# Kernel tuning notes

Hardware: AMD Instinct MI355X
Metric: run time of the kernel (lower is better)

## Reference

```python
import jax, jax.numpy as jnp
import numpy as np
import math

B, S, D, H, L, DFF = 64, 512, 512, 8, 2, 1024
DK = D // H
NEG = -1e32
LN_EPS = 1e-5


def cosine_pos_emb(seqlen, d_model):
    # pe[:,0::2]=sin(pos*div), pe[:,1::2]=cos(pos*div) -- fully overwrites the randn init
    pos = jnp.arange(seqlen, dtype=jnp.float32)[:, None]
    div = jnp.exp(jnp.arange(0, d_model, 2, dtype=jnp.float32) * (-math.log(10000.0) / d_model))
    ang = pos * div  # [S, D/2]
    return jnp.stack([jnp.sin(ang), jnp.cos(ang)], axis=-1).reshape(seqlen, d_model)


def layernorm(x, g, b):
    m = jnp.mean(x, axis=-1, keepdims=True)
    v = jnp.var(x, axis=-1, keepdims=True)
    return g * (x - m) * jax.lax.rsqrt(v + LN_EPS) + b


def setup_inputs() -> dict:
    key = jax.random.key(0)
    ks = jax.random.split(key, 8)
    sc = 0.02
    inp = {
        'q_embed_data': jax.random.normal(ks[0], (B, S, D), jnp.float32),
        'qa_embed_data': jax.random.normal(ks[1], (B, S, D), jnp.float32),
        'forget_rate': jax.random.uniform(ks[2], (B, 1, S, 1), jnp.float32),
        # per-block params, leading dim = n_blocks (kq_same=1: q uses k_linear)
        'Wk': jax.random.normal(ks[3], (L, D, D), jnp.float32) * sc,
        'bk': jnp.zeros((L, D), jnp.float32),
        'Wv': jax.random.normal(ks[4], (L, D, D), jnp.float32) * sc,
        'bv': jnp.zeros((L, D), jnp.float32),
        'Wo': jax.random.normal(ks[5], (L, D, D), jnp.float32) * sc,
        'bo': jnp.zeros((L, D), jnp.float32),
        'ln1_g': jnp.ones((L, D), jnp.float32),
        'ln1_b': jnp.zeros((L, D), jnp.float32),
        'W1': jax.random.normal(ks[6], (L, D, DFF), jnp.float32) * sc,
        'b1': jnp.zeros((L, DFF), jnp.float32),
        'W2': jax.random.normal(ks[7], (L, DFF, D), jnp.float32) * sc,
        'b2': jnp.zeros((L, D), jnp.float32),
        'ln2_g': jnp.ones((L, D), jnp.float32),
        'ln2_b': jnp.zeros((L, D), jnp.float32),
    }
    return inp


def reference(q_embed_data, qa_embed_data, forget_rate, Wk, bk, Wv, bv, Wo, bo,
              ln1_g, ln1_b, W1, b1, W2, b2, ln2_g, ln2_b):
    pe = cosine_pos_emb(S, D)
    x = q_embed_data + pe  # query/key stream
    y = qa_embed_data + pe  # value stream (fixed across blocks)
    # mask=0 path: np.triu(ones, k=0) == 0 -> strictly lower-triangular allowed
    allow = jnp.tril(jnp.ones((S, S), dtype=bool), -1)
    scale = 1.0 / math.sqrt(DK)
    for i in range(L):
        qk = (x @ Wk[i] + bk[i]).reshape(B, S, H, DK).transpose(0, 2, 1, 3)  # [B,H,S,dk]
        v = (y @ Wv[i] + bv[i]).reshape(B, S, H, DK).transpose(0, 2, 1, 3)
        scores = jnp.einsum('bhqd,bhkd->bhqk', qk, qk) * scale
        scores = scores * forget_rate  # [B,1,S,1] broadcasts over heads and keys
        scores = jnp.where(allow, scores, NEG)
        p = jax.nn.softmax(scores, axis=-1)
        p = p.at[:, :, 0, :].set(0.0)  # zero_pad: first query row zeroed
        attn = jnp.einsum('bhqk,bhkd->bhqd', p, v).transpose(0, 2, 1, 3).reshape(B, S, D)
        attn = attn @ Wo[i] + bo[i]
        x = layernorm(x + attn, ln1_g[i], ln1_b[i])
        ff = jax.nn.relu(x @ W1[i] + b1[i]) @ W2[i] + b2[i]
        x = layernorm(x + ff, ln2_g[i], ln2_b[i])
    return x
```

## Files before the change

kernel.cpp:

```cpp
#include <hip/hip_runtime.h>
#include <cstdio>

#define B_   64
#define S_   512
#define D_   512
#define H_   8
#define DK_  64
#define DFF_ 1024
#define L_   2
#define BS_  (B_ * S_)

typedef __attribute__((ext_vector_type(8))) short bf16x8;
typedef __attribute__((ext_vector_type(4))) short bf16x4;
typedef __attribute__((ext_vector_type(4))) float f32x4;

__device__ inline short f2bf(float f) {
  unsigned u = __float_as_uint(f);
  u = u + 0x7FFF + ((u >> 16) & 1);
  return (short)(u >> 16);
}
__device__ inline float bf2f(short s) {
  return __uint_as_float(((unsigned)(unsigned short)s) << 16);
}

__device__ inline void gl_lds16(const short* g, void* lds_base) {
  __builtin_amdgcn_global_load_lds(
      (const __attribute__((address_space(1))) void*)g,
      (__attribute__((address_space(3))) void*)lds_base, 16, 0, 0);
}

__global__ void pe_kernel(float* __restrict__ pe) {
  int idx = blockIdx.x * 256 + threadIdx.x;
  int s = idx >> 9, d = idx & 511;
  float dv = __expf((float)(d & ~1) * (-9.210340371976184f / (float)D_));
  float ang = (float)s * dv;
  pe[idx] = (d & 1) ? cosf(ang) : sinf(ang);
}

__global__ __launch_bounds__(256) void prep_kernel(
    const float* __restrict__ q, const float* __restrict__ qa,
    const float* __restrict__ pe, float* __restrict__ x,
    short* __restrict__ xb, short* __restrict__ yb) {
  size_t base = ((size_t)blockIdx.x * 256 + threadIdx.x) * 8;
  int sd = (int)(base & (size_t)(S_ * D_ - 1));
  f32x4 p0 = *(const f32x4*)(pe + sd);
  f32x4 p1 = *(const f32x4*)(pe + sd + 4);
  f32x4 q0 = *(const f32x4*)(q + base);
  f32x4 q1 = *(const f32x4*)(q + base + 4);
  f32x4 a0 = *(const f32x4*)(qa + base);
  f32x4 a1 = *(const f32x4*)(qa + base + 4);
  f32x4 x0, x1; bf16x8 xv, yv;
#pragma unroll
  for (int i = 0; i < 4; ++i) {
    float xe = q0[i] + p0[i]; x0[i] = xe; xv[i] = f2bf(xe);
    yv[i] = f2bf(a0[i] + p0[i]);
  }
#pragma unroll
  for (int i = 0; i < 4; ++i) {
    float xe = q1[i] + p1[i]; x1[i] = xe; xv[4 + i] = f2bf(xe);
    yv[4 + i] = f2bf(a1[i] + p1[i]);
  }
  *(f32x4*)(x + base) = x0;
  *(f32x4*)(x + base + 4) = x1;
  *(bf16x8*)(xb + base) = xv;
  *(bf16x8*)(yb + base) = yv;
}

struct TrArgs {
  const float* src[10];
  short* dst[10];
  int R[10], C[10];
};
__global__ __launch_bounds__(256) void tr_w_all(TrArgs a) {
  const int slot = blockIdx.z;
  const int R = a.R[slot], C = a.C[slot];
  const int c0 = blockIdx.x * 64, r0 = blockIdx.y * 64;
  if (c0 >= C || r0 >= R) return;
  const float* __restrict__ src = a.src[slot];
  short* __restrict__ dst = a.dst[slot];
  __shared__ short Ts[64][72];
  const int t = threadIdx.x;
#pragma unroll
  for (int it = 0; it < 2; ++it) {
    int c2 = it * 256 + t;
    int srow = c2 >> 3, schunk = c2 & 7;
    const float* sp = src + (size_t)(r0 + srow) * C + c0 + schunk * 8;
    f32x4 a0 = *(const f32x4*)sp;
    f32x4 a1 = *(const f32x4*)(sp + 4);
#pragma unroll
    for (int k = 0; k < 4; ++k) Ts[srow][schunk * 8 + k] = f2bf(a0[k]);
#pragma unroll
    for (int k = 0; k < 4; ++k) Ts[srow][schunk * 8 + 4 + k] = f2bf(a1[k]);
  }
  __syncthreads();
#pragma unroll
  for (int it = 0; it < 2; ++it) {
    int c2 = it * 256 + t;
    int orow = c2 >> 3, ochunk = c2 & 7;
    bf16x8 vv;
#pragma unroll
    for (int k = 0; k < 8; ++k) vv[k] = Ts[ochunk * 8 + k][orow];
    *(bf16x8*)(dst + (size_t)(c0 + orow) * R + r0 + ochunk * 8) = vv;
  }
}

__global__ __launch_bounds__(256, 2) void gemm_bt(
    const short* __restrict__ A, const short* __restrict__ BT,
    const float* __restrict__ bias, short* __restrict__ Cb,
    int M, int N, int K, int relu, int bias_row, int nx, int xmaj)
{
  const int nwg = gridDim.x;
  const int cpx = nwg >> 3;
  const int l = (blockIdx.x & 7) * cpx + (blockIdx.x >> 3);
  int bcol, brow;
  if (xmaj) { bcol = l % nx; brow = l / nx; }
  else      { int ny = nwg / nx; brow = l % ny; bcol = l / ny; }

  __shared__ __align__(16) short As[2][128][32];
  __shared__ __align__(16) short Bs[2][256][32];
  const int t = threadIdx.x;
  const int w = t >> 6, lane = t & 63, lr = lane & 15, lk = lane >> 4;
  const int wr = w >> 1, wc = w & 1;

  const f32x4 vzero = {0.f, 0.f, 0.f, 0.f};
  f32x4 acc[4][8];
#pragma unroll
  for (int m = 0; m < 4; ++m)
#pragma unroll
    for (int n = 0; n < 8; ++n) acc[m][n] = vzero;

  const short* Abase = A + (size_t)brow * 128 * K;
  const short* Bbase = BT + (size_t)bcol * 256 * K;

  auto stage = [&](int buf, int k0) {
#pragma unroll
    for (int it = 0; it < 2; ++it) {
      int cb = it * 256 + w * 64;
      int c = cb + lane;
      gl_lds16(Abase + (size_t)(c >> 2) * K + k0 + (c & 3) * 8, (char*)&As[buf][0][0] + (size_t)cb * 16);
    }
#pragma unroll
    for (int it = 0; it < 4; ++it) {
      int cb = it * 256 + w * 64;
      int c = cb + lane;
      gl_lds16(Bbase + (size_t)(c >> 2) * K + k0 + (c & 3) * 8, (char*)&Bs[buf][0][0] + (size_t)cb * 16);
    }
  };

  stage(0, 0);
  int cur = 0;
  for (int k0 = 0; k0 < K; k0 += 32) {
    if (k0 + 32 < K) {
      stage(cur ^ 1, k0 + 32);
      asm volatile("s_waitcnt vmcnt(6)" ::: "memory");
    } else {
      asm volatile("s_waitcnt vmcnt(0)" ::: "memory");
    }
    asm volatile("s_barrier" ::: "memory");

    bf16x8 af[4], bf[8];
#pragma unroll
    for (int m = 0; m < 4; ++m) af[m] = *(const bf16x8*)&As[cur][wr * 64 + m * 16 + lr][lk * 8];
#pragma unroll
    for (int n = 0; n < 8; ++n) bf[n] = *(const bf16x8*)&Bs[cur][wc * 128 + n * 16 + lr][lk * 8];
#pragma unroll
    for (int m = 0; m < 4; ++m)
#pragma unroll
      for (int n = 0; n < 8; ++n)
        acc[m][n] = __builtin_amdgcn_mfma_f32_16x16x32_bf16(bf[n], af[m], acc[m][n], 0, 0, 0);

    asm volatile("s_barrier" ::: "memory");
    cur ^= 1;
  }

#pragma unroll
  for (int m = 0; m < 4; ++m) {
    int row = brow * 128 + wr * 64 + m * 16 + lr;
    float brv = (bias && bias_row) ? bias[row] : 0.f;
    size_t rb = (size_t)row * N;
#pragma unroll
    for (int n = 0; n < 8; ++n) {
      int colb = bcol * 256 + wc * 128 + n * 16 + lk * 4;
      f32x4 bv4;
      if (bias && !bias_row) bv4 = *(const f32x4*)(bias + colb);
      else { bv4[0] = brv; bv4[1] = brv; bv4[2] = brv; bv4[3] = brv; }
      bf16x4 ov;
#pragma unroll
      for (int j = 0; j < 4; ++j) {
        float vv = acc[m][n][j] + bv4[j];
        if (relu) vv = fmaxf(vv, 0.f);
        ov[j] = f2bf(vv);
      }
      *(bf16x4*)(Cb + rb + colb) = ov;
    }
  }
}

template<int P>
__device__ __forceinline__ void attn_body(
    const short* __restrict__ qk, const short* __restrict__ vT,
    const float* __restrict__ fr, short* __restrict__ out,
    short (*Pl)[552], float (*redsum)[32][4],
    int h, int b, int w, int lr, int lk)
{
  constexpr int qo0 = 32 * P, qo1 = 32 * (15 - P);
  constexpr int c0 = 2 * P + 2;
  constexpr int colb1 = c0 * 16;

  const size_t qk_head = (size_t)b * S_ * D_ + (size_t)h * DK_;
  const float scale = 0.125f;

  bf16x8 qf0[2][2], qf1[2][2];
#pragma unroll
  for (int qt = 0; qt < 2; ++qt)
#pragma unroll
    for (int ks = 0; ks < 2; ++ks) {
      qf0[qt][ks] = *(const bf16x8*)(qk + qk_head + (size_t)(qo0 + qt * 16 + lr) * D_ + ks * 32 + lk * 8);
      qf1[qt][ks] = *(const bf16x8*)(qk + qk_head + (size_t)(qo1 + qt * 16 + lr) * D_ + ks * 32 + lk * 8);
    }

  float frv0[2], frv1[2];
#pragma unroll
  for (int qt = 0; qt < 2; ++qt) {
    frv0[qt] = scale * fr[(size_t)b * S_ + qo0 + qt * 16 + lr];
    frv1[qt] = scale * fr[(size_t)b * S_ + qo1 + qt * 16 + lr];
  }

  const f32x4 vzero = {0.f, 0.f, 0.f, 0.f};
  f32x4 acc[9][2];
#pragma unroll
  for (int i = 0; i < 9; ++i) { acc[i][0] = vzero; acc[i][1] = vzero; }

  const int nfr = (w < 2) ? 9 : 8;
  const short* kqbase = qk + qk_head + (size_t)lr * D_ + lk * 8;
  auto kfoff = [&](int i) -> size_t {
    int f = w + 4 * i;
    int kt = (f < c0) ? f : f - c0;
    return (size_t)kt * 16 * D_;
  };
  bf16x8 kbuf[2][2];
  {
    const short* p = kqbase + kfoff(0);
    kbuf[0][0] = *(const bf16x8*)p;
    kbuf[0][1] = *(const bf16x8*)(p + 32);
  }
#pragma unroll
  for (int i = 0; i < 9; ++i) {
    if (i < nfr) {
      if (i + 1 < nfr) {
        const short* p = kqbase + kfoff(i + 1);
        kbuf[(i + 1) & 1][0] = *(const bf16x8*)p;
        kbuf[(i + 1) & 1][1] = *(const bf16x8*)(p + 32);
      }
      const int f = w + 4 * i;
      if (f < c0) {
#pragma unroll
        for (int ks = 0; ks < 2; ++ks) {
          acc[i][0] = __builtin_amdgcn_mfma_f32_16x16x32_bf16(kbuf[i & 1][ks], qf0[0][ks], acc[i][0], 0, 0, 0);
          acc[i][1] = __builtin_amdgcn_mfma_f32_16x16x32_bf16(kbuf[i & 1][ks], qf0[1][ks], acc[i][1], 0, 0, 0);
        }
      } else {
#pragma unroll
        for (int ks = 0; ks < 2; ++ks) {
          acc[i][0] = __builtin_amdgcn_mfma_f32_16x16x32_bf16(kbuf[i & 1][ks], qf1[0][ks], acc[i][0], 0, 0, 0);
          acc[i][1] = __builtin_amdgcn_mfma_f32_16x16x32_bf16(kbuf[i & 1][ks], qf1[1][ks], acc[i][1], 0, 0, 0);
        }
      }
    }
  }

  float rs00 = 0.f, rs01 = 0.f, rs10 = 0.f, rs11 = 0.f;
#pragma unroll
  for (int frag = 0; frag < 34; ++frag) {
    if ((frag & 3) == w) {
      const int i = frag >> 2;
      const int tl = (frag < c0) ? 0 : 1;
      const int kt = tl ? frag - c0 : frag;
      const int kbase = kt * 16 + lk * 4;
      const int colb = (tl ? colb1 : 0) + kbase;
#pragma unroll
      for (int qt = 0; qt < 2; ++qt) {
        int qrow = (tl ? qo1 : qo0) + qt * 16 + lr;
        float fv = tl ? frv1[qt] : frv0[qt];
        bf16x4 pk;
        float rs = 0.f;
#pragma unroll
        for (int j = 0; j < 4; ++j) {
          float e = (kbase + j < qrow) ? __expf(acc[i][qt][j] * fv) : 0.f;
          rs += e;
          pk[j] = f2bf(e);
        }
        *(bf16x4*)&Pl[qt * 16 + lr][colb] = pk;
        if (tl == 0) { if (qt == 0) rs00 += rs; else rs01 += rs; }
        else         { if (qt == 0) rs10 += rs; else rs11 += rs; }
      }
    }
  }

#pragma unroll
  for (int msk = 16; msk < 64; msk <<= 1) {
    rs00 += __shfl_xor(rs00, msk);
    rs01 += __shfl_xor(rs01, msk);
    rs10 += __shfl_xor(rs10, msk);
    rs11 += __shfl_xor(rs11, msk);
  }
  if (lk == 0) {
    redsum[0][lr][w] = rs00;
    redsum[0][16 + lr][w] = rs01;
    redsum[1][lr][w] = rs10;
    redsum[1][16 + lr][w] = rs11;
  }
  __syncthreads();

  const int uqt0 = w & 1, udh0 = w >> 1;
  const int uqt1 = w >> 1, udh1 = w & 1;
  const short* vu0 = vT + (size_t)(h * DK_ + udh0 * 32 + lr) * BS_ + (size_t)b * S_ + lk * 8;
  const short* vu1 = vT + (size_t)(h * DK_ + udh1 * 32 + lr) * BS_ + (size_t)b * S_ + lk * 8;
  const short* prow0 = &Pl[uqt0 * 16 + lr][lk * 8];
  const short* prow1 = &Pl[uqt1 * 16 + lr][colb1 + lk * 8];

  f32x4 oacc0[2] = {vzero, vzero}, oacc1[2] = {vzero, vzero};
  bf16x8 paB[2][2];
  bf16x8 vfB[2][2][2];
  paB[0][0] = *(const bf16x8*)prow0;
  paB[0][1] = *(const bf16x8*)prow1;
#pragma unroll
  for (int n = 0; n < 2; ++n) {
    vfB[0][0][n] = *(const bf16x8*)(vu0 + (size_t)n * 16 * BS_);
    vfB[0][1][n] = *(const bf16x8*)(vu1 + (size_t)n * 16 * BS_);
  }
#pragma unroll
  for (int kb = 0; kb < 16; ++kb) {
    const int pc = kb & 1, pn = (kb + 1) & 1;
    if (kb + 1 < P + 1) {
      paB[pn][0] = *(const bf16x8*)(prow0 + (kb + 1) * 32);
#pragma unroll
      for (int n = 0; n < 2; ++n)
        vfB[pn][0][n] = *(const bf16x8*)(vu0 + (size_t)n * 16 * BS_ + (kb + 1) * 32);
    }
    if (kb + 1 < 16 - P) {
      paB[pn][1] = *(const bf16x8*)(prow1 + (kb + 1) * 32);
#pragma unroll
      for (int n = 0; n < 2; ++n)
        vfB[pn][1][n] = *(const bf16x8*)(vu1 + (size_t)n * 16 * BS_ + (kb + 1) * 32);
    }
    if (kb < P + 1) {
#pragma unroll
      for (int n = 0; n < 2; ++n)
        oacc0[n] = __builtin_amdgcn_mfma_f32_16x16x32_bf16(paB[pc][0], vfB[pc][0][n], oacc0[n], 0, 0, 0);
    }
    if (kb < 16 - P) {
#pragma unroll
      for (int n = 0; n < 2; ++n)
        oacc1[n] = __builtin_amdgcn_mfma_f32_16x16x32_bf16(paB[pc][1], vfB[pc][1][n], oacc1[n], 0, 0, 0);
    }
  }

  {
    float invd[4];
#pragma unroll
    for (int j = 0; j < 4; ++j) {
      int row = uqt0 * 16 + lk * 4 + j;
      float ds = redsum[0][row][0] + redsum[0][row][1] + redsum[0][row][2] + redsum[0][row][3];
      invd[j] = ds > 0.f ? 1.f / ds : 0.f;
    }
#pragma unroll
    for (int n = 0; n < 2; ++n)
#pragma unroll
      for (int j = 0; j < 4; ++j) {
        int qrow = qo0 + uqt0 * 16 + lk * 4 + j;
        out[qk_head + (size_t)qrow * D_ + udh0 * 32 + n * 16 + lr] = f2bf(oacc0[n][j] * invd[j]);
      }
  }
  {
    float invd[4];
#pragma unroll
    for (int j = 0; j < 4; ++j) {
      int row = uqt1 * 16 + lk * 4 + j;
      float ds = redsum[1][row][0] + redsum[1][row][1] + redsum[1][row][2] + redsum[1][row][3];
      invd[j] = ds > 0.f ? 1.f / ds : 0.f;
    }
#pragma unroll
    for (int n = 0; n < 2; ++n)
#pragma unroll
      for (int j = 0; j < 4; ++j) {
        int qrow = qo1 + uqt1 * 16 + lk * 4 + j;
        out[qk_head + (size_t)qrow * D_ + udh1 * 32 + n * 16 + lr] = f2bf(oacc1[n][j] * invd[j]);
      }
  }
}

__global__ __launch_bounds__(256, 3) void attn_kernel(
    const short* __restrict__ qk, const short* __restrict__ vT,
    const float* __restrict__ fr, short* __restrict__ out)
{
  const int hw = blockIdx.x;
  const int l = (hw & 7) * 512 + (hw >> 3);
  const int p = l & 7, hb = l >> 3;
  const int h = hb & 7, b = hb >> 3;
  const int t = threadIdx.x;
  const int w = t >> 6, lr = t & 15, lk = (t & 63) >> 4;

  __shared__ short Pl[32][552];
  __shared__ float redsum[2][32][4];

  switch (p) {
    case 0: attn_body<0>(qk, vT, fr, out, Pl, redsum, h, b, w, lr, lk); break;
    case 1: attn_body<1>(qk, vT, fr, out, Pl, redsum, h, b, w, lr, lk); break;
    case 2: attn_body<2>(qk, vT, fr, out, Pl, redsum, h, b, w, lr, lk); break;
    case 3: attn_body<3>(qk, vT, fr, out, Pl, redsum, h, b, w, lr, lk); break;
    case 4: attn_body<4>(qk, vT, fr, out, Pl, redsum, h, b, w, lr, lk); break;
    case 5: attn_body<5>(qk, vT, fr, out, Pl, redsum, h, b, w, lr, lk); break;
    case 6: attn_body<6>(qk, vT, fr, out, Pl, redsum, h, b, w, lr, lk); break;
    case 7: attn_body<7>(qk, vT, fr, out, Pl, redsum, h, b, w, lr, lk); break;
  }
}

__global__ __launch_bounds__(256) void ln_res(
    const float* __restrict__ xin, const short* __restrict__ add,
    const float* __restrict__ g, const float* __restrict__ bb,
    float* __restrict__ xout, short* __restrict__ xbout)
{
  const int row = blockIdx.x * 4 + (threadIdx.x >> 6);
  const int lane = threadIdx.x & 63;
  const size_t base = (size_t)row * D_ + lane * 8;

  f32x4 a0 = *(const f32x4*)(xin + base);
  f32x4 a1 = *(const f32x4*)(xin + base + 4);
  bf16x8 av = *(const bf16x8*)(add + base);
  float vals[8];
#pragma unroll
  for (int i = 0; i < 4; ++i) vals[i] = a0[i] + bf2f(av[i]);
#pragma unroll
  for (int i = 0; i < 4; ++i) vals[4 + i] = a1[i] + bf2f(av[4 + i]);

  float s = 0.f, sq = 0.f;
#pragma unroll
  for (int i = 0; i < 8; ++i) { s += vals[i]; sq += vals[i] * vals[i]; }
#pragma unroll
  for (int m = 1; m < 64; m <<= 1) { s += __shfl_xor(s, m); sq += __shfl_xor(sq, m); }

  float mean = s * (1.f / D_);
  float var = sq * (1.f / D_) - mean * mean;
  float rstd = rsqrtf(var + 1e-5f);

  int col = lane * 8;
  f32x4 o0, o1; bf16x8 ob;
#pragma unroll
  for (int i = 0; i < 8; ++i) {
    float vv = g[col + i] * (vals[i] - mean) * rstd + bb[col + i];
    if (i < 4) o0[i] = vv; else o1[i - 4] = vv;
    ob[i] = f2bf(vv);
  }
  *(f32x4*)(xout + base) = o0;
  *(f32x4*)(xout + base + 4) = o1;
  *(bf16x8*)(xbout + base) = ob;
}

extern "C" void kernel_launch(void* const* d_in, const int* in_sizes, int n_in,
                              void* d_out, int out_size, void* d_ws, size_t ws_size,
                              hipStream_t stream) {
  const float* q_emb = (const float*)d_in[0];
  const float* qa_emb = (const float*)d_in[1];
  const float* frate = (const float*)d_in[2];
  const float* Wk = (const float*)d_in[3];
  const float* bk = (const float*)d_in[4];
  const float* Wv = (const float*)d_in[5];
  const float* bv = (const float*)d_in[6];
  const float* Wo = (const float*)d_in[7];
  const float* bo = (const float*)d_in[8];
  const float* ln1g = (const float*)d_in[9];
  const float* ln1b = (const float*)d_in[10];
  const float* W1 = (const float*)d_in[11];
  const float* b1 = (const float*)d_in[12];
  const float* W2 = (const float*)d_in[13];
  const float* b2 = (const float*)d_in[14];
  const float* ln2g = (const float*)d_in[15];
  const float* ln2b = (const float*)d_in[16];
  float* x = (float*)d_out;

  char* ws = (char*)d_ws;
  size_t off = 0;
  auto alloc = [&](size_t bytes) -> void* {
    void* p = ws + off;
    off += (bytes + 255) & ~(size_t)255;
    return p;
  };
  const size_t MTOK = (size_t)BS_;
  float* pe    = (float*)alloc((size_t)S_ * D_ * 4);
  short* xb    = (short*)alloc(MTOK * D_ * 2);
  short* yb    = (short*)alloc(MTOK * D_ * 2);
  short* qkb   = (short*)alloc(MTOK * D_ * 2);
  short* vTb   = (short*)alloc(MTOK * D_ * 2);
  short* ff1b  = (short*)alloc(MTOK * DFF_ * 2);
  short* attnb = ff1b;
  short* goutb = qkb;
  short* wT[L_][5];
  for (int i = 0; i < L_; ++i) {
    wT[i][0] = (short*)alloc((size_t)D_ * D_ * 2);
    wT[i][1] = (short*)alloc((size_t)D_ * D_ * 2);
    wT[i][2] = (short*)alloc((size_t)D_ * D_ * 2);
    wT[i][3] = (short*)alloc((size_t)D_ * DFF_ * 2);
    wT[i][4] = (short*)alloc((size_t)DFF_ * D_ * 2);
  }
  if (off > ws_size) {
    fprintf(stderr, "parKT: workspace overflow: need %zu have %zu\n", off, ws_size);
    return;
  }

  pe_kernel<<<(S_ * D_) / 256, 256, 0, stream>>>(pe);
  prep_kernel<<<(int)(MTOK * D_ / (256 * 8)), 256, 0, stream>>>(q_emb, qa_emb, pe, x, xb, yb);

  TrArgs ta;
  for (int i = 0; i < L_; ++i) {
    ta.src[i * 5 + 0] = Wk + (size_t)i * D_ * D_;  ta.dst[i * 5 + 0] = wT[i][0]; ta.R[i * 5 + 0] = D_;   ta.C[i * 5 + 0] = D_;
    ta.src[i * 5 + 1] = Wv + (size_t)i * D_ * D_;  ta.dst[i * 5 + 1] = wT[i][1]; ta.R[i * 5 + 1] = D_;   ta.C[i * 5 + 1] = D_;
    ta.src[i * 5 + 2] = Wo + (size_t)i * D_ * D_;  ta.dst[i * 5 + 2] = wT[i][2]; ta.R[i * 5 + 2] = D_;   ta.C[i * 5 + 2] = D_;
    ta.src[i * 5 + 3] = W1 + (size_t)i * D_ * DFF_; ta.dst[i * 5 + 3] = wT[i][3]; ta.R[i * 5 + 3] = D_;   ta.C[i * 5 + 3] = DFF_;
    ta.src[i * 5 + 4] = W2 + (size_t)i * DFF_ * D_; ta.dst[i * 5 + 4] = wT[i][4]; ta.R[i * 5 + 4] = DFF_; ta.C[i * 5 + 4] = D_;
  }
  tr_w_all<<<dim3(DFF_ / 64, DFF_ / 64, 10), 256, 0, stream>>>(ta);

  const int M = (int)MTOK;
  for (int i = 0; i < L_; ++i) {
    gemm_bt<<<(M / 128) * (D_ / 256), 256, 0, stream>>>(xb, wT[i][0], bk + (size_t)i * D_, qkb, M, D_, D_, 0, 0, D_ / 256, 1);
    gemm_bt<<<(D_ / 128) * (M / 256), 256, 0, stream>>>(wT[i][1], yb, bv + (size_t)i * D_, vTb, D_, M, D_, 0, 1, M / 256, 0);
    attn_kernel<<<(S_ / 64) * H_ * B_, 256, 0, stream>>>(qkb, vTb, frate, attnb);
    gemm_bt<<<(M / 128) * (D_ / 256), 256, 0, stream>>>(attnb, wT[i][2], bo + (size_t)i * D_, goutb, M, D_, D_, 0, 0, D_ / 256, 1);
    ln_res<<<M / 4, 256, 0, stream>>>(x, goutb, ln1g + (size_t)i * D_, ln1b + (size_t)i * D_, x, xb);
    gemm_bt<<<(M / 128) * (DFF_ / 256), 256, 0, stream>>>(xb, wT[i][3], b1 + (size_t)i * DFF_, ff1b, M, DFF_, D_, 1, 0, DFF_ / 256, 1);
    gemm_bt<<<(M / 128) * (D_ / 256), 256, 0, stream>>>(ff1b, wT[i][4], b2 + (size_t)i * D_, goutb, M, D_, DFF_, 0, 0, D_ / 256, 1);
    ln_res<<<M / 4, 256, 0, stream>>>(x, goutb, ln2g + (size_t)i * D_, ln2b + (size_t)i * D_, x, xb);
  }
}
```

Before: 815.2 us.

## Carry residual stream in bf16 and prefetch V earlier in attention

Removes the fp32 residual copy of x: prep no longer writes it, and the layernorm kernels read and write only the bf16 activation, except the last one, which emits fp32 output. This cuts large fp32 read/write traffic in every residual layernorm. Separately, the attention kernel hoists V fragment loads ahead of the softmax phase and adds sched barriers to overlap loads with MFMA. The risk is reduced precision, because the residual is accumulated in bf16.

```diff
diff --git a/kernel.cpp b/kernel.cpp
--- a/kernel.cpp
+++ b/kernel.cpp
@@ -39,7 +39,7 @@
 
 __global__ __launch_bounds__(256) void prep_kernel(
     const float* __restrict__ q, const float* __restrict__ qa,
-    const float* __restrict__ pe, float* __restrict__ x,
+    const float* __restrict__ pe,
     short* __restrict__ xb, short* __restrict__ yb) {
   size_t base = ((size_t)blockIdx.x * 256 + threadIdx.x) * 8;
   int sd = (int)(base & (size_t)(S_ * D_ - 1));
@@ -49,19 +49,17 @@
   f32x4 q1 = *(const f32x4*)(q + base + 4);
   f32x4 a0 = *(const f32x4*)(qa + base);
   f32x4 a1 = *(const f32x4*)(qa + base + 4);
-  f32x4 x0, x1; bf16x8 xv, yv;
+  bf16x8 xv, yv;
 #pragma unroll
   for (int i = 0; i < 4; ++i) {
-    float xe = q0[i] + p0[i]; x0[i] = xe; xv[i] = f2bf(xe);
+    xv[i] = f2bf(q0[i] + p0[i]);
     yv[i] = f2bf(a0[i] + p0[i]);
   }
 #pragma unroll
   for (int i = 0; i < 4; ++i) {
-    float xe = q1[i] + p1[i]; x1[i] = xe; xv[4 + i] = f2bf(xe);
+    xv[4 + i] = f2bf(q1[i] + p1[i]);
     yv[4 + i] = f2bf(a1[i] + p1[i]);
   }
-  *(f32x4*)(x + base) = x0;
-  *(f32x4*)(x + base + 4) = x1;
   *(bf16x8*)(xb + base) = xv;
   *(bf16x8*)(yb + base) = yv;
 }
@@ -206,6 +204,8 @@
   constexpr int qo0 = 32 * P, qo1 = 32 * (15 - P);
   constexpr int c0 = 2 * P + 2;
   constexpr int colb1 = c0 * 16;
+  constexpr int n0 = P + 1;
+  constexpr int n1 = 16 - P;
 
   const size_t qk_head = (size_t)b * S_ * D_ + (size_t)h * DK_;
   const float scale = 0.125f;
@@ -252,6 +252,7 @@
         kbuf[(i + 1) & 1][0] = *(const bf16x8*)p;
         kbuf[(i + 1) & 1][1] = *(const bf16x8*)(p + 32);
       }
+      __builtin_amdgcn_sched_barrier(0);
       const int f = w + 4 * i;
       if (f < c0) {
 #pragma unroll
@@ -266,8 +267,29 @@
           acc[i][1] = __builtin_amdgcn_mfma_f32_16x16x32_bf16(kbuf[i & 1][ks], qf1[1][ks], acc[i][1], 0, 0, 0);
         }
       }
-    }
-  }
+      __builtin_amdgcn_sched_barrier(0);
+    }
+  }
+
+  const int uqt0 = w & 1, udh0 = w >> 1;
+  const int uqt1 = w >> 1, udh1 = w & 1;
+  const short* vu0 = vT + (size_t)(h * DK_ + udh0 * 32 + lr) * BS_ + (size_t)b * S_ + lk * 8;
+  const short* vu1 = vT + (size_t)(h * DK_ + udh1 * 32 + lr) * BS_ + (size_t)b * S_ + lk * 8;
+  bf16x8 vfB[2][2][2];
+#pragma unroll
+  for (int n = 0; n < 2; ++n) {
+    vfB[0][0][n] = *(const bf16x8*)(vu0 + (size_t)n * 16 * BS_);
+    vfB[0][1][n] = *(const bf16x8*)(vu1 + (size_t)n * 16 * BS_);
+  }
+  if (1 < n0) {
+#pragma unroll
+    for (int n = 0; n < 2; ++n)
+      vfB[1][0][n] = *(const bf16x8*)(vu0 + (size_t)n * 16 * BS_ + 32);
+  }
+#pragma unroll
+  for (int n = 0; n < 2; ++n)
+    vfB[1][1][n] = *(const bf16x8*)(vu1 + (size_t)n * 16 * BS_ + 32);
+  __builtin_amdgcn_sched_barrier(0);
 
   float rs00 = 0.f, rs01 = 0.f, rs10 = 0.f, rs11 = 0.f;
 #pragma unroll
@@ -312,48 +334,41 @@
   }
   __syncthreads();
 
-  const int uqt0 = w & 1, udh0 = w >> 1;
-  const int uqt1 = w >> 1, udh1 = w & 1;
-  const short* vu0 = vT + (size_t)(h * DK_ + udh0 * 32 + lr) * BS_ + (size_t)b * S_ + lk * 8;
-  const short* vu1 = vT + (size_t)(h * DK_ + udh1 * 32 + lr) * BS_ + (size_t)b * S_ + lk * 8;
   const short* prow0 = &Pl[uqt0 * 16 + lr][lk * 8];
   const short* prow1 = &Pl[uqt1 * 16 + lr][colb1 + lk * 8];
-
   f32x4 oacc0[2] = {vzero, vzero}, oacc1[2] = {vzero, vzero};
   bf16x8 paB[2][2];
-  bf16x8 vfB[2][2][2];
   paB[0][0] = *(const bf16x8*)prow0;
   paB[0][1] = *(const bf16x8*)prow1;
-#pragma unroll
-  for (int n = 0; n < 2; ++n) {
-    vfB[0][0][n] = *(const bf16x8*)(vu0 + (size_t)n * 16 * BS_);
-    vfB[0][1][n] = *(const bf16x8*)(vu1 + (size_t)n * 16 * BS_);
-  }
+
 #pragma unroll
   for (int kb = 0; kb < 16; ++kb) {
-    const int pc = kb & 1, pn = (kb + 1) & 1;
-    if (kb + 1 < P + 1) {
-      paB[pn][0] = *(const bf16x8*)(prow0 + (kb + 1) * 32);
-#pragma unroll
-      for (int n = 0; n < 2; ++n)
-        vfB[pn][0][n] = *(const bf16x8*)(vu0 + (size_t)n * 16 * BS_ + (kb + 1) * 32);
-    }
-    if (kb + 1 < 16 - P) {
-      paB[pn][1] = *(const bf16x8*)(prow1 + (kb + 1) * 32);
-#pragma unroll
-      for (int n = 0; n < 2; ++n)
-        vfB[pn][1][n] = *(const bf16x8*)(vu1 + (size_t)n * 16 * BS_ + (kb + 1) * 32);
-    }
-    if (kb < P + 1) {
+    const int pc = kb & 1, pn = pc ^ 1;
+    if (kb + 1 < n0) paB[pn][0] = *(const bf16x8*)(prow0 + (kb + 1) * 32);
+    if (kb + 1 < n1) paB[pn][1] = *(const bf16x8*)(prow1 + (kb + 1) * 32);
+    __builtin_amdgcn_sched_barrier(0);
+    if (kb < n0) {
 #pragma unroll
       for (int n = 0; n < 2; ++n)
         oacc0[n] = __builtin_amdgcn_mfma_f32_16x16x32_bf16(paB[pc][0], vfB[pc][0][n], oacc0[n], 0, 0, 0);
     }
-    if (kb < 16 - P) {
+    if (kb < n1) {
 #pragma unroll
       for (int n = 0; n < 2; ++n)
         oacc1[n] = __builtin_amdgcn_mfma_f32_16x16x32_bf16(paB[pc][1], vfB[pc][1][n], oacc1[n], 0, 0, 0);
     }
+    __builtin_amdgcn_sched_barrier(0);
+    if (kb + 2 < n0) {
+#pragma unroll
+      for (int n = 0; n < 2; ++n)
+        vfB[pc][0][n] = *(const bf16x8*)(vu0 + (size_t)n * 16 * BS_ + (kb + 2) * 32);
+    }
+    if (kb + 2 < n1) {
+#pragma unroll
+      for (int n = 0; n < 2; ++n)
+        vfB[pc][1][n] = *(const bf16x8*)(vu1 + (size_t)n * 16 * BS_ + (kb + 2) * 32);
+    }
+    __builtin_amdgcn_sched_barrier(0);
   }
 
   {
@@ -416,23 +431,21 @@
   }
 }
 
-__global__ __launch_bounds__(256) void ln_res(
-    const float* __restrict__ xin, const short* __restrict__ add,
+template<int FINAL>
+__global__ __launch_bounds__(256) void ln_res_t(
+    const short* __restrict__ xin, const short* __restrict__ add,
     const float* __restrict__ g, const float* __restrict__ bb,
-    float* __restrict__ xout, short* __restrict__ xbout)
+    short* __restrict__ xbout, float* __restrict__ fout)
 {
   const int row = blockIdx.x * 4 + (threadIdx.x >> 6);
   const int lane = threadIdx.x & 63;
   const size_t base = (size_t)row * D_ + lane * 8;
 
-  f32x4 a0 = *(const f32x4*)(xin + base);
-  f32x4 a1 = *(const f32x4*)(xin + base + 4);
+  bf16x8 xv = *(const bf16x8*)(xin + base);
   bf16x8 av = *(const bf16x8*)(add + base);
   float vals[8];
 #pragma unroll
-  for (int i = 0; i < 4; ++i) vals[i] = a0[i] + bf2f(av[i]);
-#pragma unroll
-  for (int i = 0; i < 4; ++i) vals[4 + i] = a1[i] + bf2f(av[4 + i]);
+  for (int i = 0; i < 8; ++i) vals[i] = bf2f(xv[i]) + bf2f(av[i]);
 
   float s = 0.f, sq = 0.f;
 #pragma unroll
@@ -445,16 +458,22 @@
   float rstd = rsqrtf(var + 1e-5f);
 
   int col = lane * 8;
-  f32x4 o0, o1; bf16x8 ob;
-#pragma unroll
-  for (int i = 0; i < 8; ++i) {
-    float vv = g[col + i] * (vals[i] - mean) * rstd + bb[col + i];
-    if (i < 4) o0[i] = vv; else o1[i - 4] = vv;
-    ob[i] = f2bf(vv);
-  }
-  *(f32x4*)(xout + base) = o0;
-  *(f32x4*)(xout + base + 4) = o1;
-  *(bf16x8*)(xbout + base) = ob;
+  if (FINAL) {
+    f32x4 o0, o1;
+#pragma unroll
+    for (int i = 0; i < 8; ++i) {
+      float vv = g[col + i] * (vals[i] - mean) * rstd + bb[col + i];
+      if (i < 4) o0[i] = vv; else o1[i - 4] = vv;
+    }
+    *(f32x4*)(fout + base) = o0;
+    *(f32x4*)(fout + base + 4) = o1;
+  } else {
+    bf16x8 ob;
+#pragma unroll
+    for (int i = 0; i < 8; ++i)
+      ob[i] = f2bf(g[col + i] * (vals[i] - mean) * rstd + bb[col + i]);
+    *(bf16x8*)(xbout + base) = ob;
+  }
 }
 
 extern "C" void kernel_launch(void* const* d_in, const int* in_sizes, int n_in,
@@ -509,7 +528,7 @@
   }
 
   pe_kernel<<<(S_ * D_) / 256, 256, 0, stream>>>(pe);
-  prep_kernel<<<(int)(MTOK * D_ / (256 * 8)), 256, 0, stream>>>(q_emb, qa_emb, pe, x, xb, yb);
+  prep_kernel<<<(int)(MTOK * D_ / (256 * 8)), 256, 0, stream>>>(q_emb, qa_emb, pe, xb, yb);
 
   TrArgs ta;
   for (int i = 0; i < L_; ++i) {
@@ -527,9 +546,12 @@
     gemm_bt<<<(D_ / 128) * (M / 256), 256, 0, stream>>>(wT[i][1], yb, bv + (size_t)i * D_, vTb, D_, M, D_, 0, 1, M / 256, 0);
     attn_kernel<<<(S_ / 64) * H_ * B_, 256, 0, stream>>>(qkb, vTb, frate, attnb);
     gemm_bt<<<(M / 128) * (D_ / 256), 256, 0, stream>>>(attnb, wT[i][2], bo + (size_t)i * D_, goutb, M, D_, D_, 0, 0, D_ / 256, 1);
-    ln_res<<<M / 4, 256, 0, stream>>>(x, goutb, ln1g + (size_t)i * D_, ln1b + (size_t)i * D_, x, xb);
+    ln_res_t<0><<<M / 4, 256, 0, stream>>>(xb, goutb, ln1g + (size_t)i * D_, ln1b + (size_t)i * D_, xb, nullptr);
     gemm_bt<<<(M / 128) * (DFF_ / 256), 256, 0, stream>>>(xb, wT[i][3], b1 + (size_t)i * DFF_, ff1b, M, DFF_, D_, 1, 0, DFF_ / 256, 1);
     gemm_bt<<<(M / 128) * (D_ / 256), 256, 0, stream>>>(ff1b, wT[i][4], b2 + (size_t)i * D_, goutb, M, D_, DFF_, 0, 0, D_ / 256, 1);
-    ln_res<<<M / 4, 256, 0, stream>>>(x, goutb, ln2g + (size_t)i * D_, ln2b + (size_t)i * D_, x, xb);
-  }
-}
+    if (i == L_ - 1)
+      ln_res_t<1><<<M / 4, 256, 0, stream>>>(xb, goutb, ln2g + (size_t)i * D_, ln2b + (size_t)i * D_, nullptr, x);
+    else
+      ln_res_t<0><<<M / 4, 256, 0, stream>>>(xb, goutb, ln2g + (size_t)i * D_, ln2b + (size_t)i * D_, xb, nullptr);
+  }
+}
```

After: 730.0 us. -10.5%, faster.
